# Optimization experiments

Measured on AMD Instinct MI355X. Metric: run time of the kernel, lower is better.

Reference implementation:

```python
import jax, jax.numpy as jnp
import numpy as np
from jax import lax

T, B, DX, H, DZ = 512, 64, 128, 256, 64
W_SCALE = 0.05


def setup_inputs() -> dict:
    key = jax.random.key(0)
    ks = jax.random.split(key, 16)
    r = lambda k, shape, s=W_SCALE: jax.random.normal(k, shape, dtype=jnp.float32) * s
    return {
        "X": jax.random.normal(ks[0], (T, B, DX), dtype=jnp.float32),
        "Wih_f": r(ks[1], (H, DX)), "Whh_f": r(ks[2], (H, H)),
        "bih_f": r(ks[3], (H,)), "bhh_f": r(ks[4], (H,)),
        "Wih_b": r(ks[5], (H, DX)), "Whh_b": r(ks[6], (H, H)),
        "bih_b": r(ks[7], (H,)), "bhh_b": r(ks[8], (H,)),
        "Wt": r(ks[9], (H, DZ)), "bt": r(ks[10], (H,)),
        "Wmu": r(ks[11], (DZ, H)), "bmu": r(ks[12], (DZ,)),
        "Wsig": r(ks[13], (DZ, H)), "bsig": r(ks[14], (DZ,)),
        "eps": jax.random.normal(ks[15], (T, B, DZ), dtype=jnp.float32),
    }


def _rnn_dir(X, Wih, Whh, bih, bhh):
    # Elman RNN (tanh): h_t = tanh(x_t Wih^T + bih + h_{t-1} Whh^T + bhh)
    xproj = jnp.einsum('tbd,hd->tbh', X, Wih) + bih + bhh  # big GEMM hoisted out of scan

    def step(h, xp):
        h = jnp.tanh(xp + h @ Whh.T)
        return h, h

    h0 = jnp.zeros((X.shape[1], Whh.shape[0]), dtype=X.dtype)
    _, hs = lax.scan(step, h0, xproj)
    return hs  # [T,B,H]


def reference(X, Wih_f, Whh_f, bih_f, bhh_f, Wih_b, Whh_b, bih_b, bhh_b,
              Wt, bt, Wmu, bmu, Wsig, bsig, eps):
    h_left = _rnn_dir(X, Wih_f, Whh_f, bih_f, bhh_f)
    h_right = _rnn_dir(X[::-1], Wih_b, Whh_b, bih_b, bhh_b)[::-1]

    def step(z_prev, inputs):
        hl, hr, eps_t = inputs
        tmp = jnp.tanh(z_prev @ Wt.T + bt)           # transition_net
        h_t = (tmp + hl + hr) * (1.0 / 3.0)
        mu = h_t @ Wmu.T + bmu
        std = jax.nn.softplus(h_t @ Wsig.T + bsig)
        z = mu + std * eps_t                         # reparameterization
        return z, (z, mu, std)

    z0 = jnp.zeros((X.shape[1], Wt.shape[1]), dtype=X.dtype)
    _, (z, mu, std) = lax.scan(step, z0, (h_left, h_right, eps))
    # stack outputs {z_post, mu_post, std_post} into one array [3,T,B,DZ]
    return jnp.stack([z, mu, std])
```

## Files before the change

kernel.cpp:

```cpp
#include <hip/hip_runtime.h>

#define TT 512
#define BB 64
#define DXX 128
#define HH 256
#define DZZ 64

typedef __attribute__((ext_vector_type(8))) short short8;
typedef __attribute__((ext_vector_type(4))) float f32x4;

#define DEV static __device__ __forceinline__

DEV unsigned short f2bf(float f){
  unsigned u = __builtin_bit_cast(unsigned, f);
  u += 0x7FFFu + ((u >> 16) & 1u);
  return (unsigned short)(u >> 16);
}
DEV unsigned pack2(float lo, float hi){
  return (unsigned)f2bf(lo) | ((unsigned)f2bf(hi) << 16);
}
DEV float bfLO(unsigned u){ return __builtin_bit_cast(float, u << 16); }
DEV float bfHI(unsigned u){ return __builtin_bit_cast(float, u & 0xffff0000u); }
DEV float ftanh(float x){
  float a = fabsf(x);
  float e = __expf(-2.f * a);
  float r = __builtin_amdgcn_rcpf(1.f + e);
  float t = (1.f - e) * r;
  return copysignf(t, x);
}
DEV float fsoftplus(float x){
  float e = __expf(fminf(x, 20.f));
  float s = __logf(1.f + e);
  return (x > 20.f) ? x : s;
}
DEV short8 pack8(const float* p){
  short8 v;
  #pragma unroll
  for (int i = 0; i < 8; ++i) v[i] = (short)f2bf(p[i]);
  return v;
}


__global__ __launch_bounds__(256, 2) void phaseA(
    const float* __restrict__ X,
    const float* __restrict__ WihF, const float* __restrict__ bihF, const float* __restrict__ bhhF,
    const float* __restrict__ WihB, const float* __restrict__ bihB, const float* __restrict__ bhhB,
    unsigned short* __restrict__ xpF)
{
  const int bid = blockIdx.x;
  const int d = bid >> 9, s = bid & 511;
  const int ts = d ? (TT - 1 - s) : s;
  const float* W  = d ? WihB : WihF;
  const float* bi = d ? bihB : bihF;
  const float* bh = d ? bhhB : bhhF;

  const int tid = threadIdx.x, q = tid >> 6, l = tid & 63;
  const int l15 = l & 15, l4 = l >> 4;

  short8 wf[4][4];
  f32x4 bias[4];
  #pragma unroll
  for (int ni = 0; ni < 4; ++ni){
    int n = 64*q + 16*ni + l15;
    #pragma unroll
    for (int ks = 0; ks < 4; ++ks)
      wf[ni][ks] = pack8(W + (size_t)n * DXX + ks*32 + l4*8);
    int n0 = 64*q + 16*ni + 4*l4;
    float4 b1 = *(const float4*)(bi + n0);
    float4 b2 = *(const float4*)(bh + n0);
    bias[ni][0]=b1.x+b2.x; bias[ni][1]=b1.y+b2.y; bias[ni][2]=b1.z+b2.z; bias[ni][3]=b1.w+b2.w;
  }

  #pragma unroll
  for (int bq = 0; bq < 4; ++bq){
    const float* xr = X + ((size_t)ts * 64 + 16*bq + l15) * DXX;
    short8 xf[4];
    #pragma unroll
    for (int ks = 0; ks < 4; ++ks) xf[ks] = pack8(xr + ks*32 + l4*8);

    f32x4 acc[4];
    #pragma unroll
    for (int ni = 0; ni < 4; ++ni) acc[ni] = bias[ni];
    #pragma unroll
    for (int ks = 0; ks < 4; ++ks)
      #pragma unroll
      for (int ni = 0; ni < 4; ++ni)
        acc[ni] = __builtin_amdgcn_mfma_f32_16x16x32_bf16(wf[ni][ks], xf[ks], acc[ni], 0, 0, 0);

    unsigned wd[8];
    #pragma unroll
    for (int ni = 0; ni < 4; ++ni){
      wd[ni*2]   = pack2(acc[ni][0], acc[ni][1]);
      wd[ni*2+1] = pack2(acc[ni][2], acc[ni][3]);
    }
    unsigned short* dst = xpF + ((((size_t)d*TT + s)*4 + bq)*4 + q)*1024 + (size_t)l*16;
    uint4 o0 = {wd[0], wd[1], wd[2], wd[3]};
    uint4 o1 = {wd[4], wd[5], wd[6], wd[7]};
    ((uint4*)dst)[0] = o0;
    ((uint4*)dst)[1] = o1;
  }
}

__global__ __launch_bounds__(256, 1) void phaseB(
    const float* __restrict__ WhhF, const float* __restrict__ WhhB,
    const unsigned short* __restrict__ xpF, unsigned short* __restrict__ hF)
{
  const int dir = blockIdx.x >> 2, bq = blockIdx.x & 3;
  const float* Whh = dir ? WhhB : WhhF;
  const int tid = threadIdx.x, q = tid >> 6, l = tid & 63;
  const int l15 = l & 15, l4 = l >> 4;
  const int swz = (l15 & 7) << 3;
  const int rbase = l15 * 256;

  __shared__ __attribute__((aligned(16))) unsigned short hbuf[2][4096];

  short8 wf[4][8];
  #pragma unroll
  for (int ni = 0; ni < 4; ++ni){
    int n = 64*q + 16*ni + l15;
    #pragma unroll
    for (int ks = 0; ks < 8; ++ks)
      wf[ni][ks] = pack8(Whh + (size_t)n * HH + ks*32 + l4*8);
  }
  for (int i = tid; i < 2048; i += 256) ((unsigned*)hbuf[0])[i] = 0u;

  const size_t strideS = 16384;
  const size_t laneOff = (size_t)bq*4096 + (size_t)q*1024 + (size_t)l*16;
  const unsigned short* xpP = xpF + (size_t)dir*TT*strideS + laneOff;
  unsigned short* hD = hF + (size_t)dir*TT*strideS + laneOff;

  uint4 xq0, xq1;
  { const uint4* src = (const uint4*)xpP; xq0 = src[0]; xq1 = src[1]; }

  uint4 p0, p1;
  size_t prevOff = 0;
  __syncthreads();

  for (int s = 0; s < TT; ++s){
    if (s > 0){
      *(uint4*)(hD + prevOff)     = p0;
      *(uint4*)(hD + prevOff + 8) = p1;
    }
    uint4 xn0, xn1;
    {
      int sn = (s + 1 < TT) ? s + 1 : s;
      const uint4* src = (const uint4*)(xpP + (size_t)sn * strideS);
      xn0 = src[0]; xn1 = src[1];
    }
    f32x4 acc[4];
    {
      unsigned W8[8] = {xq0.x, xq0.y, xq0.z, xq0.w, xq1.x, xq1.y, xq1.z, xq1.w};
      #pragma unroll
      for (int ni = 0; ni < 4; ++ni){
        acc[ni][0] = bfLO(W8[ni*2]);   acc[ni][1] = bfHI(W8[ni*2]);
        acc[ni][2] = bfLO(W8[ni*2+1]); acc[ni][3] = bfHI(W8[ni*2+1]);
      }
    }
    const unsigned short* hb = hbuf[s & 1];
    #pragma unroll
    for (int ks = 0; ks < 8; ++ks){
      short8 b = *(const short8*)(hb + ((rbase + ks*32 + l4*8) ^ swz));
      #pragma unroll
      for (int ni = 0; ni < 4; ++ni)
        acc[ni] = __builtin_amdgcn_mfma_f32_16x16x32_bf16(wf[ni][ks], b, acc[ni], 0, 0, 0);
    }
    unsigned short* hw = hbuf[(s & 1) ^ 1];
    unsigned wd[8];
    #pragma unroll
    for (int ni = 0; ni < 4; ++ni){
      float t0 = ftanh(acc[ni][0]), t1 = ftanh(acc[ni][1]);
      float t2 = ftanh(acc[ni][2]), t3 = ftanh(acc[ni][3]);
      unsigned lo = pack2(t0, t1), hi = pack2(t2, t3);
      wd[ni*2] = lo; wd[ni*2+1] = hi;
      int ea = rbase + ((64*q + 16*ni + 4*l4) ^ swz);
      uint2 v; v.x = lo; v.y = hi;
      *(uint2*)(hw + ea) = v;
    }
    p0.x=wd[0]; p0.y=wd[1]; p0.z=wd[2]; p0.w=wd[3];
    p1.x=wd[4]; p1.y=wd[5]; p1.z=wd[6]; p1.w=wd[7];
    prevOff = (size_t)(dir ? (TT - 1 - s) : s) * strideS;
    xq0 = xn0; xq1 = xn1;
    __syncthreads();
  }
  *(uint4*)(hD + prevOff)     = p0;
  *(uint4*)(hD + prevOff + 8) = p1;
}

__global__ __launch_bounds__(256, 1) void phaseC(
    const float* __restrict__ Wt,  const float* __restrict__ bt,
    const float* __restrict__ Wmu, const float* __restrict__ bmu,
    const float* __restrict__ Wsig,const float* __restrict__ bsig,
    const float* __restrict__ eps, const unsigned short* __restrict__ hF,
    float* __restrict__ out)
{
  const int bq = blockIdx.x;
  const int tid = threadIdx.x, q = tid >> 6, l = tid & 63;
  const int l15 = l & 15, l4 = l >> 4;
  const int swz = (l15 & 7) << 3;
  const int rbase = l15 * 256;
  const int zrbase = l15 * 64;

  __shared__ __attribute__((aligned(16))) unsigned short zbuf[1024];
  __shared__ __attribute__((aligned(16))) unsigned short hbuf[4096];

  short8 wtf[4][2]; f32x4 btb[4];
  #pragma unroll
  for (int ni = 0; ni < 4; ++ni){
    int n = 64*q + 16*ni + l15;
    #pragma unroll
    for (int ks = 0; ks < 2; ++ks)
      wtf[ni][ks] = pack8(Wt + (size_t)n * DZZ + ks*32 + l4*8);
    float4 b4 = *(const float4*)(bt + 64*q + 16*ni + 4*l4);
    btb[ni][0]=b4.x; btb[ni][1]=b4.y; btb[ni][2]=b4.z; btb[ni][3]=b4.w;
  }
  short8 wm[8], wsg[8];
  {
    int r = 16*q + l15;
    #pragma unroll
    for (int ks = 0; ks < 8; ++ks){
      wm[ks]  = pack8(Wmu  + (size_t)r * HH + ks*32 + l4*8);
      wsg[ks] = pack8(Wsig + (size_t)r * HH + ks*32 + l4*8);
    }
  }
  f32x4 bm4, bs4;
  {
    float4 a = *(const float4*)(bmu  + 16*q + 4*l4);
    float4 b = *(const float4*)(bsig + 16*q + 4*l4);
    bm4[0]=a.x; bm4[1]=a.y; bm4[2]=a.z; bm4[3]=a.w;
    bs4[0]=b.x; bs4[1]=b.y; bs4[2]=b.z; bs4[3]=b.w;
  }
  for (int i = tid; i < 512; i += 256) ((unsigned*)zbuf)[i] = 0u;

  const size_t strideS = 16384;
  const size_t laneOff = (size_t)bq*4096 + (size_t)q*1024 + (size_t)l*16;
  const unsigned short* hLp = hF + laneOff;
  const unsigned short* hRp = hLp + (size_t)TT * strideS;
  const float* eP = eps + ((size_t)(16*bq + l15)) * 64 + 16*q + 4*l4;

  uint4 hl0, hl1, hr0, hr1; f32x4 ef;
  {
    const uint4* sl = (const uint4*)hLp;
    const uint4* sr = (const uint4*)hRp;
    hl0 = sl[0]; hl1 = sl[1]; hr0 = sr[0]; hr1 = sr[1];
    float4 e4 = *(const float4*)eP;
    ef[0]=e4.x; ef[1]=e4.y; ef[2]=e4.z; ef[3]=e4.w;
  }
  const size_t TBZ = (size_t)TT * 64 * 64;
  f32x4 dz, dmu, dsp;
  size_t obPrev = 0;
  __syncthreads();

  for (int t = 0; t < TT; ++t){
    if (t > 0){
      *(float4*)(out + obPrev)         = *(float4*)&dz;
      *(float4*)(out + TBZ + obPrev)   = *(float4*)&dmu;
      *(float4*)(out + 2*TBZ + obPrev) = *(float4*)&dsp;
    }
    uint4 nl0, nl1, nr0, nr1; f32x4 nef;
    {
      int tn = (t + 1 < TT) ? t + 1 : t;
      const uint4* sl = (const uint4*)(hLp + (size_t)tn*strideS);
      const uint4* sr = (const uint4*)(hRp + (size_t)tn*strideS);
      nl0 = sl[0]; nl1 = sl[1]; nr0 = sr[0]; nr1 = sr[1];
      float4 e4 = *(const float4*)(eP + (size_t)tn*4096);
      nef[0]=e4.x; nef[1]=e4.y; nef[2]=e4.z; nef[3]=e4.w;
    }
    f32x4 at[4];
    #pragma unroll
    for (int ni = 0; ni < 4; ++ni) at[ni] = btb[ni];
    #pragma unroll
    for (int ks = 0; ks < 2; ++ks){
      short8 b = *(const short8*)(zbuf + ((zrbase + ks*32 + l4*8) ^ swz));
      #pragma unroll
      for (int ni = 0; ni < 4; ++ni)
        at[ni] = __builtin_amdgcn_mfma_f32_16x16x32_bf16(wtf[ni][ks], b, at[ni], 0, 0, 0);
    }
    {
      unsigned HL[8] = {hl0.x, hl0.y, hl0.z, hl0.w, hl1.x, hl1.y, hl1.z, hl1.w};
      unsigned HR[8] = {hr0.x, hr0.y, hr0.z, hr0.w, hr1.x, hr1.y, hr1.z, hr1.w};
      #pragma unroll
      for (int ni = 0; ni < 4; ++ni){
        unsigned wl0 = HL[ni*2], wl1 = HL[ni*2+1];
        unsigned wr0 = HR[ni*2], wr1 = HR[ni*2+1];
        float h0 = (ftanh(at[ni][0]) + bfLO(wl0) + bfLO(wr0)) * (1.f/3.f);
        float h1 = (ftanh(at[ni][1]) + bfHI(wl0) + bfHI(wr0)) * (1.f/3.f);
        float h2 = (ftanh(at[ni][2]) + bfLO(wl1) + bfLO(wr1)) * (1.f/3.f);
        float h3 = (ftanh(at[ni][3]) + bfHI(wl1) + bfHI(wr1)) * (1.f/3.f);
        int ea = rbase + ((64*q + 16*ni + 4*l4) ^ swz);
        uint2 v; v.x = pack2(h0, h1); v.y = pack2(h2, h3);
        *(uint2*)(hbuf + ea) = v;
      }
    }
    __syncthreads();

    f32x4 a0 = bm4, s0 = bs4;
    f32x4 a1 = {0.f,0.f,0.f,0.f}, s1 = {0.f,0.f,0.f,0.f};
    #pragma unroll
    for (int ks = 0; ks < 4; ++ks){
      short8 b = *(const short8*)(hbuf + ((rbase + ks*32 + l4*8) ^ swz));
      a0 = __builtin_amdgcn_mfma_f32_16x16x32_bf16(wm[ks],  b, a0, 0, 0, 0);
      s0 = __builtin_amdgcn_mfma_f32_16x16x32_bf16(wsg[ks], b, s0, 0, 0, 0);
    }
    #pragma unroll
    for (int ks = 4; ks < 8; ++ks){
      short8 b = *(const short8*)(hbuf + ((rbase + ks*32 + l4*8) ^ swz));
      a1 = __builtin_amdgcn_mfma_f32_16x16x32_bf16(wm[ks],  b, a1, 0, 0, 0);
      s1 = __builtin_amdgcn_mfma_f32_16x16x32_bf16(wsg[ks], b, s1, 0, 0, 0);
    }
    f32x4 mu = a0 + a1;
    f32x4 sg = s0 + s1;
    #pragma unroll
    for (int reg = 0; reg < 4; ++reg){
      float sp = fsoftplus(sg[reg]);
      float zv = __builtin_fmaf(sp, ef[reg], mu[reg]);
      dz[reg] = zv; dmu[reg] = mu[reg]; dsp[reg] = sp;
    }
    {
      int zea = zrbase + ((16*q + 4*l4) ^ swz);
      uint2 v; v.x = pack2(dz[0], dz[1]); v.y = pack2(dz[2], dz[3]);
      *(uint2*)(zbuf + zea) = v;
    }
    obPrev = ((size_t)t*64 + 16*bq + l15)*64 + 16*q + 4*l4;
    hl0 = nl0; hl1 = nl1; hr0 = nr0; hr1 = nr1; ef = nef;
    __syncthreads();
  }
  *(float4*)(out + obPrev)         = *(float4*)&dz;
  *(float4*)(out + TBZ + obPrev)   = *(float4*)&dmu;
  *(float4*)(out + 2*TBZ + obPrev) = *(float4*)&dsp;
}

extern "C" void kernel_launch(void* const* d_in, const int* in_sizes, int n_in,
                              void* d_out, int out_size, void* d_ws, size_t ws_size,
                              hipStream_t stream)
{
  const float* X      = (const float*)d_in[0];
  const float* Wih_f  = (const float*)d_in[1];
  const float* Whh_f  = (const float*)d_in[2];
  const float* bih_f  = (const float*)d_in[3];
  const float* bhh_f  = (const float*)d_in[4];
  const float* Wih_b  = (const float*)d_in[5];
  const float* Whh_b  = (const float*)d_in[6];
  const float* bih_b  = (const float*)d_in[7];
  const float* bhh_b  = (const float*)d_in[8];
  const float* Wt     = (const float*)d_in[9];
  const float* bt     = (const float*)d_in[10];
  const float* Wmu    = (const float*)d_in[11];
  const float* bmu    = (const float*)d_in[12];
  const float* Wsig   = (const float*)d_in[13];
  const float* bsig   = (const float*)d_in[14];
  const float* eps    = (const float*)d_in[15];

  unsigned short* xpF = (unsigned short*)d_ws;
  unsigned short* hF  = xpF + (size_t)2 * TT * 16384;

  phaseA<<<dim3(1024), dim3(256), 0, stream>>>(X, Wih_f, bih_f, bhh_f, Wih_b, bih_b, bhh_b, xpF);
  phaseB<<<dim3(8), dim3(256), 0, stream>>>(Whh_f, Whh_b, xpF, hF);
  phaseC<<<dim3(4), dim3(256), 0, stream>>>(Wt, bt, Wmu, bmu, Wsig, bsig, eps, hF, (float*)d_out);
}
```

Before: 1.272 ms.

## Unroll recurrent loops by two with deeper prefetch and LDS-only barriers

Phase B and phase C sequential loops are unrolled by two, with static double-buffer selection and global prefetch of xproj, hidden states and eps two steps ahead in separate register sets. Barriers are replaced by a custom s_waitcnt lgkmcnt(0) plus s_barrier, so outstanding global loads and stores need not drain at each step. The phase B MFMA chain is split into two independent accumulators to shorten the dependency chain, and LDS fragment reads are hoisted ahead of the MFMAs. These changes target the per-step latency of the serial recurrence, at the cost of more registers and reliance on the weaker barrier being correct, since it no longer waits on outstanding global memory operations.

```diff
diff --git a/kernel.cpp b/kernel.cpp
--- a/kernel.cpp
+++ b/kernel.cpp
@@ -10,6 +10,7 @@
 typedef __attribute__((ext_vector_type(4))) float f32x4;
 
 #define DEV static __device__ __forceinline__
+#define MFMA(a,b,c) __builtin_amdgcn_mfma_f32_16x16x32_bf16((a),(b),(c),0,0,0)
 
 DEV unsigned short f2bf(float f){
   unsigned u = __builtin_bit_cast(unsigned, f);
@@ -38,6 +39,12 @@
   #pragma unroll
   for (int i = 0; i < 8; ++i) v[i] = (short)f2bf(p[i]);
   return v;
+}
+DEV void barrier_lgkm(){
+  asm volatile("s_waitcnt lgkmcnt(0)" ::: "memory");
+  __builtin_amdgcn_sched_barrier(0);
+  __builtin_amdgcn_s_barrier();
+  __builtin_amdgcn_sched_barrier(0);
 }
 
 
@@ -85,7 +92,7 @@
     for (int ks = 0; ks < 4; ++ks)
       #pragma unroll
       for (int ni = 0; ni < 4; ++ni)
-        acc[ni] = __builtin_amdgcn_mfma_f32_16x16x32_bf16(wf[ni][ks], xf[ks], acc[ni], 0, 0, 0);
+        acc[ni] = MFMA(wf[ni][ks], xf[ks], acc[ni]);
 
     unsigned wd[8];
     #pragma unroll
@@ -129,58 +136,67 @@
   const unsigned short* xpP = xpF + (size_t)dir*TT*strideS + laneOff;
   unsigned short* hD = hF + (size_t)dir*TT*strideS + laneOff;
 
-  uint4 xq0, xq1;
-  { const uint4* src = (const uint4*)xpP; xq0 = src[0]; xq1 = src[1]; }
-
-  uint4 p0, p1;
+  uint4 xqA0, xqA1, xqB0, xqB1;
+  { const uint4* p = (const uint4*)xpP;             xqA0 = p[0]; xqA1 = p[1]; }
+  { const uint4* p = (const uint4*)(xpP + strideS); xqB0 = p[0]; xqB1 = p[1]; }
+
+  uint4 p0 = {0,0,0,0}, p1 = {0,0,0,0};
   size_t prevOff = 0;
-  __syncthreads();
-
-  for (int s = 0; s < TT; ++s){
-    if (s > 0){
-      *(uint4*)(hD + prevOff)     = p0;
-      *(uint4*)(hD + prevOff + 8) = p1;
-    }
-    uint4 xn0, xn1;
-    {
-      int sn = (s + 1 < TT) ? s + 1 : s;
+  barrier_lgkm();
+
+  auto bstep = [&](int s, uint4& XQ0, uint4& XQ1,
+                   const unsigned short* RD, unsigned short* WR){
+    short8 b[8];
+    #pragma unroll
+    for (int ks = 0; ks < 8; ++ks)
+      b[ks] = *(const short8*)(RD + ((rbase + ks*32 + l4*8) ^ swz));
+    *(uint4*)(hD + prevOff)     = p0;
+    *(uint4*)(hD + prevOff + 8) = p1;
+    f32x4 accE[4], accO[4];
+    {
+      unsigned W8[8] = {XQ0.x, XQ0.y, XQ0.z, XQ0.w, XQ1.x, XQ1.y, XQ1.z, XQ1.w};
+      #pragma unroll
+      for (int ni = 0; ni < 4; ++ni){
+        accE[ni][0] = bfLO(W8[ni*2]);   accE[ni][1] = bfHI(W8[ni*2]);
+        accE[ni][2] = bfLO(W8[ni*2+1]); accE[ni][3] = bfHI(W8[ni*2+1]);
+        accO[ni][0] = 0.f; accO[ni][1] = 0.f; accO[ni][2] = 0.f; accO[ni][3] = 0.f;
+      }
+    }
+    {
+      int sn = (s + 2 < TT) ? s + 2 : TT - 1;
       const uint4* src = (const uint4*)(xpP + (size_t)sn * strideS);
-      xn0 = src[0]; xn1 = src[1];
-    }
-    f32x4 acc[4];
-    {
-      unsigned W8[8] = {xq0.x, xq0.y, xq0.z, xq0.w, xq1.x, xq1.y, xq1.z, xq1.w};
+      XQ0 = src[0]; XQ1 = src[1];
+    }
+    #pragma unroll
+    for (int ks = 0; ks < 8; ks += 2){
       #pragma unroll
       for (int ni = 0; ni < 4; ++ni){
-        acc[ni][0] = bfLO(W8[ni*2]);   acc[ni][1] = bfHI(W8[ni*2]);
-        acc[ni][2] = bfLO(W8[ni*2+1]); acc[ni][3] = bfHI(W8[ni*2+1]);
+        accE[ni] = MFMA(wf[ni][ks],   b[ks],   accE[ni]);
+        accO[ni] = MFMA(wf[ni][ks+1], b[ks+1], accO[ni]);
       }
     }
-    const unsigned short* hb = hbuf[s & 1];
-    #pragma unroll
-    for (int ks = 0; ks < 8; ++ks){
-      short8 b = *(const short8*)(hb + ((rbase + ks*32 + l4*8) ^ swz));
-      #pragma unroll
-      for (int ni = 0; ni < 4; ++ni)
-        acc[ni] = __builtin_amdgcn_mfma_f32_16x16x32_bf16(wf[ni][ks], b, acc[ni], 0, 0, 0);
-    }
-    unsigned short* hw = hbuf[(s & 1) ^ 1];
     unsigned wd[8];
     #pragma unroll
     for (int ni = 0; ni < 4; ++ni){
-      float t0 = ftanh(acc[ni][0]), t1 = ftanh(acc[ni][1]);
-      float t2 = ftanh(acc[ni][2]), t3 = ftanh(acc[ni][3]);
+      float t0 = ftanh(accE[ni][0] + accO[ni][0]);
+      float t1 = ftanh(accE[ni][1] + accO[ni][1]);
+      float t2 = ftanh(accE[ni][2] + accO[ni][2]);
+      float t3 = ftanh(accE[ni][3] + accO[ni][3]);
       unsigned lo = pack2(t0, t1), hi = pack2(t2, t3);
       wd[ni*2] = lo; wd[ni*2+1] = hi;
       int ea = rbase + ((64*q + 16*ni + 4*l4) ^ swz);
       uint2 v; v.x = lo; v.y = hi;
-      *(uint2*)(hw + ea) = v;
+      *(uint2*)(WR + ea) = v;
     }
     p0.x=wd[0]; p0.y=wd[1]; p0.z=wd[2]; p0.w=wd[3];
     p1.x=wd[4]; p1.y=wd[5]; p1.z=wd[6]; p1.w=wd[7];
     prevOff = (size_t)(dir ? (TT - 1 - s) : s) * strideS;
-    xq0 = xn0; xq1 = xn1;
-    __syncthreads();
+    barrier_lgkm();
+  };
+
+  for (int s = 0; s < TT; s += 2){
+    bstep(s,     xqA0, xqA1, hbuf[0], hbuf[1]);
+    bstep(s + 1, xqB0, xqB1, hbuf[1], hbuf[0]);
   }
   *(uint4*)(hD + prevOff)     = p0;
   *(uint4*)(hD + prevOff + 8) = p1;
@@ -237,51 +253,46 @@
   const unsigned short* hRp = hLp + (size_t)TT * strideS;
   const float* eP = eps + ((size_t)(16*bq + l15)) * 64 + 16*q + 4*l4;
 
-  uint4 hl0, hl1, hr0, hr1; f32x4 ef;
+  uint4 hlA0, hlA1, hrA0, hrA1, hlB0, hlB1, hrB0, hrB1;
+  f32x4 efA, efB;
   {
-    const uint4* sl = (const uint4*)hLp;
-    const uint4* sr = (const uint4*)hRp;
-    hl0 = sl[0]; hl1 = sl[1]; hr0 = sr[0]; hr1 = sr[1];
-    float4 e4 = *(const float4*)eP;
-    ef[0]=e4.x; ef[1]=e4.y; ef[2]=e4.z; ef[3]=e4.w;
+    const uint4* sl = (const uint4*)hLp;              hlA0 = sl[0]; hlA1 = sl[1];
+    const uint4* sr = (const uint4*)hRp;              hrA0 = sr[0]; hrA1 = sr[1];
+    const uint4* tl = (const uint4*)(hLp + strideS);  hlB0 = tl[0]; hlB1 = tl[1];
+    const uint4* tr = (const uint4*)(hRp + strideS);  hrB0 = tr[0]; hrB1 = tr[1];
+    float4 e0 = *(const float4*)eP;
+    float4 e1 = *(const float4*)(eP + 4096);
+    efA[0]=e0.x; efA[1]=e0.y; efA[2]=e0.z; efA[3]=e0.w;
+    efB[0]=e1.x; efB[1]=e1.y; efB[2]=e1.z; efB[3]=e1.w;
   }
   const size_t TBZ = (size_t)TT * 64 * 64;
-  f32x4 dz, dmu, dsp;
-  size_t obPrev = 0;
-  __syncthreads();
-
-  for (int t = 0; t < TT; ++t){
-    if (t > 0){
-      *(float4*)(out + obPrev)         = *(float4*)&dz;
-      *(float4*)(out + TBZ + obPrev)   = *(float4*)&dmu;
-      *(float4*)(out + 2*TBZ + obPrev) = *(float4*)&dsp;
-    }
-    uint4 nl0, nl1, nr0, nr1; f32x4 nef;
-    {
-      int tn = (t + 1 < TT) ? t + 1 : t;
-      const uint4* sl = (const uint4*)(hLp + (size_t)tn*strideS);
-      const uint4* sr = (const uint4*)(hRp + (size_t)tn*strideS);
-      nl0 = sl[0]; nl1 = sl[1]; nr0 = sr[0]; nr1 = sr[1];
-      float4 e4 = *(const float4*)(eP + (size_t)tn*4096);
-      nef[0]=e4.x; nef[1]=e4.y; nef[2]=e4.z; nef[3]=e4.w;
-    }
+  f32x4 dz = {0.f,0.f,0.f,0.f}, dmu = {0.f,0.f,0.f,0.f}, dsp = {0.f,0.f,0.f,0.f};
+  size_t obPrev = ((size_t)16*bq + l15)*64 + 16*q + 4*l4;
+  barrier_lgkm();
+
+  auto cstep = [&](int t, uint4& HL0, uint4& HL1, uint4& HR0, uint4& HR1, f32x4& EF){
+    short8 zb[2];
+    #pragma unroll
+    for (int ks = 0; ks < 2; ++ks)
+      zb[ks] = *(const short8*)(zbuf + ((zrbase + ks*32 + l4*8) ^ swz));
+    *(float4*)(out + obPrev)         = *(float4*)&dz;
+    *(float4*)(out + TBZ + obPrev)   = *(float4*)&dmu;
+    *(float4*)(out + 2*TBZ + obPrev) = *(float4*)&dsp;
     f32x4 at[4];
     #pragma unroll
     for (int ni = 0; ni < 4; ++ni) at[ni] = btb[ni];
     #pragma unroll
-    for (int ks = 0; ks < 2; ++ks){
-      short8 b = *(const short8*)(zbuf + ((zrbase + ks*32 + l4*8) ^ swz));
+    for (int ks = 0; ks < 2; ++ks)
       #pragma unroll
       for (int ni = 0; ni < 4; ++ni)
-        at[ni] = __builtin_amdgcn_mfma_f32_16x16x32_bf16(wtf[ni][ks], b, at[ni], 0, 0, 0);
-    }
-    {
-      unsigned HL[8] = {hl0.x, hl0.y, hl0.z, hl0.w, hl1.x, hl1.y, hl1.z, hl1.w};
-      unsigned HR[8] = {hr0.x, hr0.y, hr0.z, hr0.w, hr1.x, hr1.y, hr1.z, hr1.w};
+        at[ni] = MFMA(wtf[ni][ks], zb[ks], at[ni]);
+    {
+      unsigned HLw[8] = {HL0.x, HL0.y, HL0.z, HL0.w, HL1.x, HL1.y, HL1.z, HL1.w};
+      unsigned HRw[8] = {HR0.x, HR0.y, HR0.z, HR0.w, HR1.x, HR1.y, HR1.z, HR1.w};
       #pragma unroll
       for (int ni = 0; ni < 4; ++ni){
-        unsigned wl0 = HL[ni*2], wl1 = HL[ni*2+1];
-        unsigned wr0 = HR[ni*2], wr1 = HR[ni*2+1];
+        unsigned wl0 = HLw[ni*2], wl1 = HLw[ni*2+1];
+        unsigned wr0 = HRw[ni*2], wr1 = HRw[ni*2+1];
         float h0 = (ftanh(at[ni][0]) + bfLO(wl0) + bfLO(wr0)) * (1.f/3.f);
         float h1 = (ftanh(at[ni][1]) + bfHI(wl0) + bfHI(wr0)) * (1.f/3.f);
         float h2 = (ftanh(at[ni][2]) + bfLO(wl1) + bfLO(wr1)) * (1.f/3.f);
@@ -291,28 +302,40 @@
         *(uint2*)(hbuf + ea) = v;
       }
     }
-    __syncthreads();
-
-    f32x4 a0 = bm4, s0 = bs4;
-    f32x4 a1 = {0.f,0.f,0.f,0.f}, s1 = {0.f,0.f,0.f,0.f};
+    {
+      int tn = (t + 2 < TT) ? t + 2 : TT - 1;
+      const uint4* sl = (const uint4*)(hLp + (size_t)tn*strideS);
+      const uint4* sr = (const uint4*)(hRp + (size_t)tn*strideS);
+      HL0 = sl[0]; HL1 = sl[1]; HR0 = sr[0]; HR1 = sr[1];
+    }
+    barrier_lgkm();
+
+    short8 hbl[4];
+    #pragma unroll
+    for (int ks = 0; ks < 4; ++ks)
+      hbl[ks] = *(const short8*)(hbuf + ((rbase + ks*32 + l4*8) ^ swz));
+    f32x4 am0 = bm4, as0 = bs4;
     #pragma unroll
     for (int ks = 0; ks < 4; ++ks){
-      short8 b = *(const short8*)(hbuf + ((rbase + ks*32 + l4*8) ^ swz));
-      a0 = __builtin_amdgcn_mfma_f32_16x16x32_bf16(wm[ks],  b, a0, 0, 0, 0);
-      s0 = __builtin_amdgcn_mfma_f32_16x16x32_bf16(wsg[ks], b, s0, 0, 0, 0);
-    }
-    #pragma unroll
-    for (int ks = 4; ks < 8; ++ks){
-      short8 b = *(const short8*)(hbuf + ((rbase + ks*32 + l4*8) ^ swz));
-      a1 = __builtin_amdgcn_mfma_f32_16x16x32_bf16(wm[ks],  b, a1, 0, 0, 0);
-      s1 = __builtin_amdgcn_mfma_f32_16x16x32_bf16(wsg[ks], b, s1, 0, 0, 0);
-    }
-    f32x4 mu = a0 + a1;
-    f32x4 sg = s0 + s1;
+      am0 = MFMA(wm[ks],  hbl[ks], am0);
+      as0 = MFMA(wsg[ks], hbl[ks], as0);
+    }
+    short8 hbh[4];
+    #pragma unroll
+    for (int ks = 0; ks < 4; ++ks)
+      hbh[ks] = *(const short8*)(hbuf + ((rbase + (ks+4)*32 + l4*8) ^ swz));
+    f32x4 am1 = {0.f,0.f,0.f,0.f}, as1 = {0.f,0.f,0.f,0.f};
+    #pragma unroll
+    for (int ks = 0; ks < 4; ++ks){
+      am1 = MFMA(wm[ks+4],  hbh[ks], am1);
+      as1 = MFMA(wsg[ks+4], hbh[ks], as1);
+    }
+    f32x4 mu = am0 + am1;
+    f32x4 sg = as0 + as1;
     #pragma unroll
     for (int reg = 0; reg < 4; ++reg){
       float sp = fsoftplus(sg[reg]);
-      float zv = __builtin_fmaf(sp, ef[reg], mu[reg]);
+      float zv = __builtin_fmaf(sp, EF[reg], mu[reg]);
       dz[reg] = zv; dmu[reg] = mu[reg]; dsp[reg] = sp;
     }
     {
@@ -320,9 +343,18 @@
       uint2 v; v.x = pack2(dz[0], dz[1]); v.y = pack2(dz[2], dz[3]);
       *(uint2*)(zbuf + zea) = v;
     }
+    {
+      int tn = (t + 2 < TT) ? t + 2 : TT - 1;
+      float4 e4 = *(const float4*)(eP + (size_t)tn*4096);
+      EF[0]=e4.x; EF[1]=e4.y; EF[2]=e4.z; EF[3]=e4.w;
+    }
     obPrev = ((size_t)t*64 + 16*bq + l15)*64 + 16*q + 4*l4;
-    hl0 = nl0; hl1 = nl1; hr0 = nr0; hr1 = nr1; ef = nef;
-    __syncthreads();
+    barrier_lgkm();
+  };
+
+  for (int t = 0; t < TT; t += 2){
+    cstep(t,     hlA0, hlA1, hrA0, hrA1, efA);
+    cstep(t + 1, hlB0, hlB1, hrB0, hrB1, efB);
   }
   *(float4*)(out + obPrev)         = *(float4*)&dz;
   *(float4*)(out + TBZ + obPrev)   = *(float4*)&dmu;
```

New measurement: 1.247 ms. -2.0%, faster.
